# Optimization experiments

Hardware: AMD Instinct MI355X
Metric: run time of the kernel (lower is better)

Reference implementation:

```python
import jax, jax.numpy as jnp
import numpy as np
import math

B, C, H, W = 8, 512, 32, 32
NUM_GROUPS = 32
NUM_HEADS = C // 64  # num_head_channels=64 -> 8 heads
EPS = 1e-5


def setup_inputs() -> dict:
    key = jax.random.key(0)
    ks = jax.random.split(key, 7)
    x = jax.random.normal(ks[0], (B, C, H, W), dtype=jnp.float32)
    gn_w = jax.random.uniform(ks[1], (C,), dtype=jnp.float32, minval=0.5, maxval=1.5)
    gn_b = jax.random.normal(ks[2], (C,), dtype=jnp.float32) * 0.1
    qkv_w = jax.random.normal(ks[3], (3 * C, C), dtype=jnp.float32) * 0.02
    qkv_b = jax.random.normal(ks[4], (3 * C,), dtype=jnp.float32) * 0.02
    proj_w = jax.random.normal(ks[5], (C, C), dtype=jnp.float32) * 0.02
    proj_b = jax.random.normal(ks[6], (C,), dtype=jnp.float32) * 0.02
    return {"x": x, "gn_w": gn_w, "gn_b": gn_b, "qkv_w": qkv_w,
            "qkv_b": qkv_b, "proj_w": proj_w, "proj_b": proj_b}


def _group_norm(x, w, b):
    # x: [B, C, L]
    bb, cc, ll = x.shape
    g = x.reshape(bb, NUM_GROUPS, cc // NUM_GROUPS, ll)
    mean = g.mean(axis=(2, 3), keepdims=True)
    var = g.var(axis=(2, 3), keepdims=True)
    g = (g - mean) * jax.lax.rsqrt(var + EPS)
    return g.reshape(bb, cc, ll) * w[None, :, None] + b[None, :, None]


def reference(x, gn_w, gn_b, qkv_w, qkv_b, proj_w, proj_b):
    b, c, h, w = x.shape
    L = h * w
    xf = x.reshape(b, c, L)
    # 1x1 conv1d QKV on normalized input: weight [3C, C]
    qkv = jnp.einsum('oc,bcl->bol', qkv_w, _group_norm(xf, gn_w, gn_b)) + qkv_b[None, :, None]
    ch = c // NUM_HEADS  # per-head channels
    qkv = qkv.reshape(b * NUM_HEADS, 3 * ch, L)
    q, k, v = qkv[:, :ch], qkv[:, ch:2 * ch], qkv[:, 2 * ch:]
    scale = 1.0 / math.sqrt(math.sqrt(ch))
    # [b*H, T, S] scores, softmax over source dim (computed in fp32 per source)
    weight = jnp.einsum('bct,bcs->bts', q * scale, k * scale)
    weight = jax.nn.softmax(weight.astype(jnp.float32), axis=-1).astype(weight.dtype)
    a = jnp.einsum('bts,bcs->bct', weight, v).reshape(b, c, L)
    hproj = jnp.einsum('oc,bcl->bol', proj_w, a) + proj_b[None, :, None]
    return (xf + hproj).reshape(b, c, h, w)
```

## Files before the change

kernel.cpp:

```cpp
#include <hip/hip_runtime.h>
#include <math.h>

#define BB 8
#define CC 512
#define LL 1024
#define GG 32
#define CPG 16
#define NH 8
#define CH 64

typedef unsigned short ushort_t;
typedef __attribute__((ext_vector_type(8))) short short8;
typedef __attribute__((ext_vector_type(4))) float f32x4;
typedef __attribute__((ext_vector_type(16))) float f32x16;

#define SCALE_Q 0.18033688f

__device__ inline ushort_t f2bf(float f) {
  union { float f; unsigned u; } v;
  v.f = f;
  unsigned r = v.u + 0x7FFFu + ((v.u >> 16) & 1u);
  return (ushort_t)(r >> 16);
}

__device__ inline unsigned pack_bf2(float lo, float hi) {
  return __builtin_amdgcn_perm(__float_as_uint(hi), __float_as_uint(lo),
                               0x07060302u);
}

__device__ inline int swz(int r, int k) {
  return r * 64 + ((((k >> 3) ^ (r & 7)) << 3) | (k & 7));
}

__device__ __forceinline__ void g2l16(const void* g, void* l) {
  __builtin_amdgcn_global_load_lds((const unsigned int*)g, (unsigned int*)l,
                                   16, 0, 0);
}

__global__ __launch_bounds__(256) void pre_kernel(
    const float* __restrict__ x, const float* __restrict__ gn_w,
    const float* __restrict__ gn_b, const float* __restrict__ qkv_w,
    const float* __restrict__ proj_w, float* __restrict__ s_bc,
    float* __restrict__ t_bc, ushort_t* __restrict__ wq,
    ushort_t* __restrict__ wp) {
  if (blockIdx.x < BB * GG) {
    int b = blockIdx.x / GG;
    int g = blockIdx.x % GG;
    const float4* xg4 =
        (const float4*)(x + ((size_t)b * CC + (size_t)g * CPG) * LL);
    float sum = 0.f, sq = 0.f;
#pragma unroll
    for (int i = 0; i < 16; ++i) {
      float4 v = xg4[threadIdx.x + i * 256];
      sum += (v.x + v.y) + (v.z + v.w);
      sq += (v.x * v.x + v.y * v.y) + (v.z * v.z + v.w * v.w);
    }
#pragma unroll
    for (int off = 32; off > 0; off >>= 1) {
      sum += __shfl_down(sum, off);
      sq += __shfl_down(sq, off);
    }
    __shared__ float red[8];
    __shared__ float st[2];
    int wave = threadIdx.x >> 6;
    if ((threadIdx.x & 63) == 0) {
      red[wave] = sum;
      red[4 + wave] = sq;
    }
    __syncthreads();
    if (threadIdx.x == 0) {
      float s = red[0] + red[1] + red[2] + red[3];
      float q = red[4] + red[5] + red[6] + red[7];
      float mean = s * (1.f / (CPG * LL));
      float var = q * (1.f / (CPG * LL)) - mean * mean;
      st[0] = mean;
      st[1] = rsqrtf(var + 1e-5f);
    }
    __syncthreads();
    if (threadIdx.x < CPG) {
      int c = g * CPG + threadIdx.x;
      float w = gn_w[c];
      float sc = st[1] * w;
      s_bc[b * CC + c] = sc;
      t_bc[b * CC + c] = gn_b[c] - st[0] * sc;
    }
  } else {
    int cb = blockIdx.x - BB * GG;
    int idx = (cb * 256 + threadIdx.x) * 4;
    const int N1 = 3 * CC * CC;
    float4 v;
    ushort_t* mat;
    int row, k;
    if (idx < N1) {
      v = *(const float4*)(qkv_w + idx);
      row = idx >> 9;
      k = idx & 511;
      mat = wq + (size_t)row * CC;
    } else {
      int j = idx - N1;
      v = *(const float4*)(proj_w + j);
      row = j >> 9;
      k = j & 511;
      mat = wp + (size_t)row * CC;
    }
    int dcol = (k & ~63) | ((((k >> 3) & 7) ^ (row & 7)) << 3) | (k & 7);
    unsigned lo = f2bf(v.x) | ((unsigned)f2bf(v.y) << 16);
    unsigned hi = f2bf(v.z) | ((unsigned)f2bf(v.w) << 16);
    *(uint2*)(mat + dcol) = make_uint2(lo, hi);
  }
}

__global__ __launch_bounds__(256) void xnt_kernel(
    const float* __restrict__ x, const float* __restrict__ s_bc,
    const float* __restrict__ t_bc, ushort_t* __restrict__ xnT) {
  const int b = blockIdx.z;
  const int c0 = blockIdx.y * 64;
  const int l0 = blockIdx.x * 64;
  const int tid = threadIdx.x;
  __shared__ ushort_t Ts[64 * 72];
#pragma unroll
  for (int r4 = 0; r4 < 4; ++r4) {
    int c_local = (tid >> 4) + r4 * 16;
    int l_local = (tid & 15) * 4;
    int c = c0 + c_local;
    float sc = s_bc[b * CC + c], sh = t_bc[b * CC + c];
    float4 v = *(const float4*)(x + ((size_t)b * CC + c) * LL + l0 + l_local);
    float vv[4] = {v.x, v.y, v.z, v.w};
#pragma unroll
    for (int dl = 0; dl < 4; ++dl) {
      int l = l_local + dl;
      int cs = c_local ^ (((l >> 2) & 7) << 3);
      Ts[l * 72 + cs] = f2bf(vv[dl] * sc + sh);
    }
  }
  __syncthreads();
#pragma unroll
  for (int rep = 0; rep < 2; ++rep) {
    int gid = tid + rep * 256;
    int l = gid >> 3, seg = gid & 7;
    uint4 v = *(const uint4*)&Ts[l * 72 + ((seg * 8) ^ (((l >> 2) & 7) << 3))];
    *(uint4*)(xnT + ((size_t)b * LL + l0 + l) * CC + c0 +
              ((seg ^ (l & 7)) << 3)) = v;
  }
}

__global__ __launch_bounds__(384, 3) void qkv_mfma_kernel(
    const ushort_t* __restrict__ wq, const ushort_t* __restrict__ xnT,
    const float* __restrict__ qkv_b, ushort_t* __restrict__ qT,
    ushort_t* __restrict__ kT, ushort_t* __restrict__ vbuf) {
  const int b = blockIdx.z;
  const int m0 = blockIdx.y * 192;
  const int n0 = blockIdx.x * 128;
  const int tid = threadIdx.x;
  const int w = tid >> 6, lane = tid & 63;
  const int col = lane & 15, quad = lane >> 4;
  const int wm = (w >> 1) * 64, wn = (w & 1) * 64;
  __shared__ ushort_t Smem[2 * 20480];
  f32x4 acc[4][4];
  f32x4 z = {0.f, 0.f, 0.f, 0.f};
#pragma unroll
  for (int i = 0; i < 4; ++i)
#pragma unroll
    for (int j = 0; j < 4; ++j) acc[i][j] = z;

  const ushort_t* arow = wq + (size_t)m0 * CC;
  const ushort_t* brow = xnT + ((size_t)b * LL + n0) * CC;

  auto stage = [&](int bb, int k0) {
    ushort_t* As = Smem + bb * 20480;
    ushort_t* Bs = As + 12288;
#pragma unroll
    for (int j = 0; j < 4; ++j) {
      int e = (j * 6 + w) * 512 + lane * 8;
      g2l16(arow + (size_t)(e >> 6) * CC + k0 + (e & 63),
            As + (j * 6 + w) * 512);
    }
    if (w < 4) {
#pragma unroll
      for (int j = 0; j < 4; ++j) {
        int e = (j * 4 + w) * 512 + lane * 8;
        g2l16(brow + (size_t)(e >> 6) * CC + k0 + (e & 63),
              Bs + (j * 4 + w) * 512);
      }
    }
  };

  stage(0, 0);
  __syncthreads();
  int cur = 0;
  for (int step = 0; step < 8; ++step) {
    if (step < 7) stage(cur ^ 1, (step + 1) * 64);
    const ushort_t* As = Smem + cur * 20480;
    const ushort_t* Bs = As + 12288;
#pragma unroll
    for (int kk = 0; kk < 2; ++kk) {
      short8 af[4], bf[4];
#pragma unroll
      for (int mi = 0; mi < 4; ++mi)
        af[mi] = *(const short8*)&As[swz(wm + mi * 16 + col, kk * 32 + quad * 8)];
#pragma unroll
      for (int ni = 0; ni < 4; ++ni)
        bf[ni] = *(const short8*)&Bs[swz(wn + ni * 16 + col, kk * 32 + quad * 8)];
#pragma unroll
      for (int mi = 0; mi < 4; ++mi)
#pragma unroll
        for (int ni = 0; ni < 4; ++ni)
          acc[mi][ni] = __builtin_amdgcn_mfma_f32_16x16x32_bf16(
              af[mi], bf[ni], acc[mi][ni], 0, 0, 0);
    }
    __syncthreads();
    cur ^= 1;
  }
  const int ci_w = w >> 1;
  ushort_t* Tile = Smem + ci_w * 8192;
  if (ci_w < 2) {
    const float sc = (ci_w == 0) ? SCALE_Q : 1.f;
#pragma unroll
    for (int mi = 0; mi < 4; ++mi) {
      int mg = m0 + wm + mi * 16 + quad * 4;
      float b0 = qkv_b[mg + 0], b1 = qkv_b[mg + 1];
      float b2 = qkv_b[mg + 2], b3 = qkv_b[mg + 3];
      int ch = mi * 16 + quad * 4;
#pragma unroll
      for (int ni = 0; ni < 4; ++ni) {
        int lloc = wn + ni * 16 + col;
        float v0 = (acc[mi][ni][0] + b0) * sc;
        float v1 = (acc[mi][ni][1] + b1) * sc;
        float v2 = (acc[mi][ni][2] + b2) * sc;
        float v3 = (acc[mi][ni][3] + b3) * sc;
        int chs = ch ^ ((lloc & 7) << 3);
        *(uint2*)&Tile[lloc * 64 + chs] =
            make_uint2(pack_bf2(v0, v1), pack_bf2(v2, v3));
      }
    }
  } else {
#pragma unroll
    for (int mi = 0; mi < 4; ++mi)
#pragma unroll
      for (int r = 0; r < 4; ++r) {
        int ch = mi * 16 + quad * 4 + r;
        float bias = qkv_b[m0 + wm + ch];
#pragma unroll
        for (int ni = 0; ni < 4; ++ni) {
          int lloc = wn + ni * 16 + col;
          Tile[ch * 128 + lloc] =
              (ushort_t)(__float_as_uint(acc[mi][ni][r] + bias) >> 16);
        }
      }
  }
  __syncthreads();
  const int head = blockIdx.y;
  const int bh = b * NH + head;
#pragma unroll
  for (int ci = 0; ci < 3; ++ci) {
    ushort_t* T2 = Smem + ci * 8192;
    if (ci < 2) {
      ushort_t* dst = (ci == 0) ? qT : kT;
#pragma unroll
      for (int it = 0; it < 3; ++it) {
        int idx = tid + it * 384;
        if (idx < 1024) {
          int l = idx >> 3, seg = idx & 7;
          uint4 v = *(const uint4*)&T2[l * 64 + seg * 8];
          *(uint4*)(dst + ((size_t)bh * LL + n0 + l) * CH + seg * 8) = v;
        }
      }
    } else {
#pragma unroll
      for (int it = 0; it < 3; ++it) {
        int idx = tid + it * 384;
        if (idx < 1024) {
          int ch = idx >> 4, lseg = idx & 15;
          uint4 v = *(const uint4*)&T2[ch * 128 + lseg * 8];
          int g = lseg & 7, blk = lseg >> 3;
          *(uint4*)(vbuf + ((size_t)bh * CH + ch) * LL + n0 + blk * 64 +
                    ((g ^ (ch & 7)) << 3)) = v;
        }
      }
    }
  }
}

__global__ __launch_bounds__(256) void attn_mfma_kernel(
    const ushort_t* __restrict__ qT, const ushort_t* __restrict__ kT,
    const ushort_t* __restrict__ vbuf, ushort_t* __restrict__ abuf) {
  const int Bx = blockIdx.x;
  const int bh = (Bx & 7) * 8 + ((Bx >> 3) >> 3);
  const int t0g = ((Bx >> 3) & 7) * 128;
  const int b = bh >> 3, h = bh & 7;
  const int tid = threadIdx.x;
  const int w = tid >> 6, lane = tid & 63;
  const int ln31 = lane & 31, hi = lane >> 5;
  __shared__ ushort_t Ksm[2][64 * 64];
  __shared__ ushort_t Vsm[2][64 * 64];

  const ushort_t* kbase = kT + (size_t)bh * LL * CH;
  const ushort_t* vbase = vbuf + (size_t)bh * CH * LL;
  const int eb = w * 1024 + lane * 8;

#pragma unroll
  for (int i = 0; i < 2; ++i) {
    int ee = eb + i * 512;
    g2l16(kbase + ee, &Ksm[0][w * 1024 + i * 512]);
    g2l16(vbase + (size_t)(ee >> 6) * LL + (ee & 63),
          &Vsm[0][w * 1024 + i * 512]);
  }
  const ushort_t* qtile = qT + ((size_t)bh * LL + t0g) * CH;
  short8 bq[4];
#pragma unroll
  for (int j = 0; j < 4; ++j)
    bq[j] = *(const short8*)&qtile[swz(w * 32 + ln31, j * 16 + hi * 8)];

  float m_s = 0.f, lsum = 0.f;
  f32x16 oacc[2];
  f32x16 zz = {0.f, 0.f, 0.f, 0.f, 0.f, 0.f, 0.f, 0.f,
               0.f, 0.f, 0.f, 0.f, 0.f, 0.f, 0.f, 0.f};
  oacc[0] = zz;
  oacc[1] = zz;
  __syncthreads();

  int cur = 0;
  for (int it = 0; it < 16; ++it) {
    if (it < 15) {
      const ushort_t* kn = kbase + (size_t)(it + 1) * 64 * CH;
      const ushort_t* vn = vbase + (it + 1) * 64;
#pragma unroll
      for (int i = 0; i < 2; ++i) {
        int ee = eb + i * 512;
        g2l16(kn + ee, &Ksm[cur ^ 1][w * 1024 + i * 512]);
        g2l16(vn + (size_t)(ee >> 6) * LL + (ee & 63),
              &Vsm[cur ^ 1][w * 1024 + i * 512]);
      }
    }
    const ushort_t* Kc = Ksm[cur];
    const ushort_t* Vc = Vsm[cur];
    f32x16 sacc[2];
    sacc[0] = zz;
    sacc[1] = zz;
    __builtin_amdgcn_s_setprio(1);
#pragma unroll
    for (int sq = 0; sq < 2; ++sq)
#pragma unroll
      for (int j = 0; j < 4; ++j) {
        short8 ak = *(const short8*)&Kc[swz(sq * 32 + ln31, j * 16 + hi * 8)];
        sacc[sq] = __builtin_amdgcn_mfma_f32_32x32x16_bf16(ak, bq[j],
                                                           sacc[sq], 0, 0, 0);
      }
    __builtin_amdgcn_s_setprio(0);
    if (it == 0) {
      float mx = sacc[0][0];
#pragma unroll
      for (int sq = 0; sq < 2; ++sq)
#pragma unroll
        for (int r = 0; r < 16; ++r) mx = fmaxf(mx, sacc[sq][r]);
#pragma unroll
      for (int off = 32; off > 0; off >>= 1) mx = fmaxf(mx, __shfl_xor(mx, off));
      m_s = mx;
    }
    short8 pf[4];
#pragma unroll
    for (int sq = 0; sq < 2; ++sq) {
      float p[16];
#pragma unroll
      for (int r = 0; r < 16; ++r) {
        p[r] = __builtin_amdgcn_exp2f(sacc[sq][r] - m_s);
        lsum += p[r];
      }
      unsigned d0[4], d1[4];
#pragma unroll
      for (int q = 0; q < 4; ++q) {
        d0[q] = pack_bf2(p[q * 4 + 0], p[q * 4 + 1]);
        d1[q] = pack_bf2(p[q * 4 + 2], p[q * 4 + 3]);
      }
#pragma unroll
      for (int m = 0; m < 2; ++m) {
        unsigned x0 = d0[m * 2], y0 = d0[m * 2 + 1];
        unsigned x1 = d1[m * 2], y1 = d1[m * 2 + 1];
        asm volatile("v_permlane32_swap_b32 %0, %1" : "+v"(x0), "+v"(y0));
        asm volatile("v_permlane32_swap_b32 %0, %1" : "+v"(x1), "+v"(y1));
        union { uint4 u; short8 s; } fu;
        fu.u = make_uint4(x0, x1, y0, y1);
        pf[sq * 2 + m] = fu.s;
      }
    }
    __builtin_amdgcn_s_setprio(1);
#pragma unroll
    for (int cq = 0; cq < 2; ++cq)
#pragma unroll
      for (int ks = 0; ks < 4; ++ks) {
        short8 bv = *(const short8*)&Vc[swz(cq * 32 + ln31, ks * 16 + hi * 8)];
        oacc[cq] = __builtin_amdgcn_mfma_f32_32x32x16_bf16(pf[ks], bv,
                                                           oacc[cq], 0, 0, 0);
      }
    __builtin_amdgcn_s_setprio(0);
    __syncthreads();
    cur ^= 1;
  }
  lsum += __shfl_xor(lsum, 32);
#pragma unroll
  for (int r = 0; r < 16; ++r) {
    int tl = (r & 3) + 8 * (r >> 2) + 4 * hi;
    float li = 1.f / __shfl(lsum, tl, 64);
    int lg = t0g + w * 32 + tl;
#pragma unroll
    for (int cq = 0; cq < 2; ++cq) {
      int cl = cq * 32 + ln31;
      int dcol = ((((cl >> 3) ^ (lg & 7)) << 3) | (cl & 7));
      abuf[((size_t)b * LL + lg) * CC + h * CH + dcol] =
          f2bf(oacc[cq][r] * li);
    }
  }
}

__global__ __launch_bounds__(256) void proj_mfma_kernel(
    const ushort_t* __restrict__ wp, const ushort_t* __restrict__ abuf,
    const float* __restrict__ proj_b, const float* __restrict__ x,
    float* __restrict__ out) {
  const int b = blockIdx.z;
  const int m0 = blockIdx.y * 64;
  const int n0 = blockIdx.x * 128;
  const int tid = threadIdx.x;
  const int w = tid >> 6, lane = tid & 63;
  const int col = lane & 15, quad = lane >> 4;
  const int wm = (w >> 1) * 32, wn = (w & 1) * 64;
  __shared__ ushort_t Smem[2 * 12288];
  f32x4 acc[2][4];
  f32x4 z = {0.f, 0.f, 0.f, 0.f};
#pragma unroll
  for (int i = 0; i < 2; ++i)
#pragma unroll
    for (int j = 0; j < 4; ++j) acc[i][j] = z;

  const ushort_t* arow = wp + (size_t)m0 * CC;
  const ushort_t* brow = abuf + ((size_t)b * LL + n0) * CC;

  auto stage = [&](int bb, int k0) {
    ushort_t* As = Smem + bb * 12288;
    ushort_t* Bs = As + 4096;
#pragma unroll
    for (int j = 0; j < 2; ++j) {
      int e = (j * 4 + w) * 512 + lane * 8;
      g2l16(arow + (size_t)(e >> 6) * CC + k0 + (e & 63),
            As + (j * 4 + w) * 512);
    }
#pragma unroll
    for (int j = 0; j < 4; ++j) {
      int e = (j * 4 + w) * 512 + lane * 8;
      g2l16(brow + (size_t)(e >> 6) * CC + k0 + (e & 63),
            Bs + (j * 4 + w) * 512);
    }
  };

  stage(0, 0);
  __syncthreads();
  int cur = 0;
  for (int step = 0; step < 8; ++step) {
    if (step < 7) stage(cur ^ 1, (step + 1) * 64);
    const ushort_t* As = Smem + cur * 12288;
    const ushort_t* Bs = As + 4096;
#pragma unroll
    for (int kk = 0; kk < 2; ++kk) {
      short8 af[2], bf[4];
#pragma unroll
      for (int mi = 0; mi < 2; ++mi)
        af[mi] = *(const short8*)&As[swz(wm + mi * 16 + col, kk * 32 + quad * 8)];
#pragma unroll
      for (int ni = 0; ni < 4; ++ni)
        bf[ni] = *(const short8*)&Bs[swz(wn + ni * 16 + col, kk * 32 + quad * 8)];
#pragma unroll
      for (int mi = 0; mi < 2; ++mi)
#pragma unroll
        for (int ni = 0; ni < 4; ++ni)
          acc[mi][ni] = __builtin_amdgcn_mfma_f32_16x16x32_bf16(
              af[mi], bf[ni], acc[mi][ni], 0, 0, 0);
    }
    __syncthreads();
    cur ^= 1;
  }
#pragma unroll
  for (int mi = 0; mi < 2; ++mi)
#pragma unroll
    for (int r = 0; r < 4; ++r) {
      int o = m0 + wm + mi * 16 + quad * 4 + r;
      float bias = proj_b[o];
#pragma unroll
      for (int ni = 0; ni < 4; ++ni) {
        int l = n0 + wn + ni * 16 + col;
        size_t off = ((size_t)b * CC + o) * LL + l;
        out[off] = x[off] + bias + acc[mi][ni][r];
      }
    }
}

extern "C" void kernel_launch(void* const* d_in, const int* in_sizes, int n_in,
                              void* d_out, int out_size, void* d_ws,
                              size_t ws_size, hipStream_t stream) {
  const float* x = (const float*)d_in[0];
  const float* gn_w = (const float*)d_in[1];
  const float* gn_b = (const float*)d_in[2];
  const float* qkv_w = (const float*)d_in[3];
  const float* qkv_b = (const float*)d_in[4];
  const float* proj_w = (const float*)d_in[5];
  const float* proj_b = (const float*)d_in[6];
  float* out = (float*)d_out;

  char* ws = (char*)d_ws;
  float* s_bc = (float*)ws;
  float* t_bc = s_bc + BB * CC;
  ushort_t* wq = (ushort_t*)(t_bc + BB * CC);
  ushort_t* wp = wq + (size_t)3 * CC * CC;
  ushort_t* xnT = wp + (size_t)CC * CC;
  ushort_t* qT = xnT + (size_t)BB * LL * CC;
  ushort_t* kT = qT + (size_t)BB * NH * LL * CH;
  ushort_t* vb = kT + (size_t)BB * NH * LL * CH;
  ushort_t* abuf = vb + (size_t)BB * NH * LL * CH;

  pre_kernel<<<BB * GG + 1024, 256, 0, stream>>>(x, gn_w, gn_b, qkv_w, proj_w,
                                                 s_bc, t_bc, wq, wp);
  xnt_kernel<<<dim3(LL / 64, CC / 64, BB), 256, 0, stream>>>(x, s_bc, t_bc,
                                                             xnT);
  qkv_mfma_kernel<<<dim3(LL / 128, 1536 / 192, BB), 384, 0, stream>>>(
      wq, xnT, qkv_b, qT, kT, vb);
  attn_mfma_kernel<<<dim3(512), 256, 0, stream>>>(qT, kT, vb, abuf);
  proj_mfma_kernel<<<dim3(LL / 128, CC / 64, BB), 256, 0, stream>>>(
      wp, abuf, proj_b, x, out);
}
```

Before: 139.5 us.

## Fuse group-norm stats with normalize-transpose and double attention query tile per block

```diff
diff --git a/kernel.cpp b/kernel.cpp
--- a/kernel.cpp
+++ b/kernel.cpp
@@ -37,56 +37,85 @@
                                    16, 0, 0);
 }
 
-__global__ __launch_bounds__(256) void pre_kernel(
+__global__ __launch_bounds__(512) void gnx_kernel(
     const float* __restrict__ x, const float* __restrict__ gn_w,
     const float* __restrict__ gn_b, const float* __restrict__ qkv_w,
-    const float* __restrict__ proj_w, float* __restrict__ s_bc,
-    float* __restrict__ t_bc, ushort_t* __restrict__ wq,
-    ushort_t* __restrict__ wp) {
+    const float* __restrict__ proj_w, ushort_t* __restrict__ xnT,
+    ushort_t* __restrict__ wq, ushort_t* __restrict__ wp) {
   if (blockIdx.x < BB * GG) {
-    int b = blockIdx.x / GG;
-    int g = blockIdx.x % GG;
-    const float4* xg4 =
-        (const float4*)(x + ((size_t)b * CC + (size_t)g * CPG) * LL);
+    const int b = blockIdx.x / GG;
+    const int g = blockIdx.x % GG;
+    const int tid = threadIdx.x;
+    const int ch = tid >> 5;
+    const int lseg = tid & 31;
+    __shared__ ushort_t Ts[1024 * 32];
+    __shared__ float red[16];
+    __shared__ float st[2];
+    const float* xc = x + ((size_t)b * CC + (size_t)g * CPG + ch) * LL;
+    float4 v[8];
     float sum = 0.f, sq = 0.f;
 #pragma unroll
-    for (int i = 0; i < 16; ++i) {
-      float4 v = xg4[threadIdx.x + i * 256];
-      sum += (v.x + v.y) + (v.z + v.w);
-      sq += (v.x * v.x + v.y * v.y) + (v.z * v.z + v.w * v.w);
+    for (int i = 0; i < 8; ++i) {
+      v[i] = *(const float4*)(xc + lseg * 32 + i * 4);
+      sum += (v[i].x + v[i].y) + (v[i].z + v[i].w);
+      sq += (v[i].x * v[i].x + v[i].y * v[i].y) +
+            (v[i].z * v[i].z + v[i].w * v[i].w);
     }
 #pragma unroll
     for (int off = 32; off > 0; off >>= 1) {
       sum += __shfl_down(sum, off);
       sq += __shfl_down(sq, off);
     }
-    __shared__ float red[8];
-    __shared__ float st[2];
-    int wave = threadIdx.x >> 6;
-    if ((threadIdx.x & 63) == 0) {
+    const int wave = tid >> 6;
+    if ((tid & 63) == 0) {
       red[wave] = sum;
-      red[4 + wave] = sq;
+      red[8 + wave] = sq;
     }
     __syncthreads();
-    if (threadIdx.x == 0) {
-      float s = red[0] + red[1] + red[2] + red[3];
-      float q = red[4] + red[5] + red[6] + red[7];
+    if (tid == 0) {
+      float s = 0.f, q = 0.f;
+#pragma unroll
+      for (int i = 0; i < 8; ++i) {
+        s += red[i];
+        q += red[8 + i];
+      }
       float mean = s * (1.f / (CPG * LL));
       float var = q * (1.f / (CPG * LL)) - mean * mean;
       st[0] = mean;
       st[1] = rsqrtf(var + 1e-5f);
     }
     __syncthreads();
-    if (threadIdx.x < CPG) {
-      int c = g * CPG + threadIdx.x;
-      float w = gn_w[c];
-      float sc = st[1] * w;
-      s_bc[b * CC + c] = sc;
-      t_bc[b * CC + c] = gn_b[c] - st[0] * sc;
+    const int c = g * CPG + ch;
+    const float sc = st[1] * gn_w[c];
+    const float sh = gn_b[c] - st[0] * sc;
+    const int chG = ch >> 3, ch7 = ch & 7;
+#pragma unroll
+    for (int i = 0; i < 8; ++i) {
+      float vv[4] = {v[i].x, v[i].y, v[i].z, v[i].w};
+#pragma unroll
+      for (int j = 0; j < 4; ++j) {
+        int l = lseg * 32 + i * 4 + j;
+        int key = ((l >> 5) + (l >> 2)) & 3;
+        int slot = (chG + key) & 3;
+        Ts[l * 32 + slot * 8 + ch7] = f2bf(vv[j] * sc + sh);
+      }
+    }
+    __syncthreads();
+    const int cb64 = (g >> 2) * 64;
+    const int grpb = (g & 3) * 2;
+#pragma unroll
+    for (int it = 0; it < 4; ++it) {
+      int idx = tid + it * 512;
+      int l = idx >> 1, gsel = idx & 1;
+      int key = ((l >> 5) + (l >> 2)) & 3;
+      int slot = (gsel + key) & 3;
+      uint4 val = *(const uint4*)&Ts[l * 32 + slot * 8];
+      int grp = (grpb + gsel) ^ (l & 7);
+      *(uint4*)(xnT + ((size_t)b * LL + l) * CC + cb64 + grp * 8) = val;
     }
   } else {
     int cb = blockIdx.x - BB * GG;
-    int idx = (cb * 256 + threadIdx.x) * 4;
+    int idx = (cb * 512 + threadIdx.x) * 4;
     const int N1 = 3 * CC * CC;
     float4 v;
     ushort_t* mat;
@@ -110,40 +139,6 @@
   }
 }
 
-__global__ __launch_bounds__(256) void xnt_kernel(
-    const float* __restrict__ x, const float* __restrict__ s_bc,
-    const float* __restrict__ t_bc, ushort_t* __restrict__ xnT) {
-  const int b = blockIdx.z;
-  const int c0 = blockIdx.y * 64;
-  const int l0 = blockIdx.x * 64;
-  const int tid = threadIdx.x;
-  __shared__ ushort_t Ts[64 * 72];
-#pragma unroll
-  for (int r4 = 0; r4 < 4; ++r4) {
-    int c_local = (tid >> 4) + r4 * 16;
-    int l_local = (tid & 15) * 4;
-    int c = c0 + c_local;
-    float sc = s_bc[b * CC + c], sh = t_bc[b * CC + c];
-    float4 v = *(const float4*)(x + ((size_t)b * CC + c) * LL + l0 + l_local);
-    float vv[4] = {v.x, v.y, v.z, v.w};
-#pragma unroll
-    for (int dl = 0; dl < 4; ++dl) {
-      int l = l_local + dl;
-      int cs = c_local ^ (((l >> 2) & 7) << 3);
-      Ts[l * 72 + cs] = f2bf(vv[dl] * sc + sh);
-    }
-  }
-  __syncthreads();
-#pragma unroll
-  for (int rep = 0; rep < 2; ++rep) {
-    int gid = tid + rep * 256;
-    int l = gid >> 3, seg = gid & 7;
-    uint4 v = *(const uint4*)&Ts[l * 72 + ((seg * 8) ^ (((l >> 2) & 7) << 3))];
-    *(uint4*)(xnT + ((size_t)b * LL + l0 + l) * CC + c0 +
-              ((seg ^ (l & 7)) << 3)) = v;
-  }
-}
-
 __global__ __launch_bounds__(384, 3) void qkv_mfma_kernel(
     const ushort_t* __restrict__ wq, const ushort_t* __restrict__ xnT,
     const float* __restrict__ qkv_b, ushort_t* __restrict__ qT,
@@ -281,12 +276,12 @@
   }
 }
 
-__global__ __launch_bounds__(256) void attn_mfma_kernel(
+__global__ __launch_bounds__(512) void attn_mfma_kernel(
     const ushort_t* __restrict__ qT, const ushort_t* __restrict__ kT,
     const ushort_t* __restrict__ vbuf, ushort_t* __restrict__ abuf) {
   const int Bx = blockIdx.x;
-  const int bh = (Bx & 7) * 8 + ((Bx >> 3) >> 3);
-  const int t0g = ((Bx >> 3) & 7) * 128;
+  const int bh = (Bx & 7) * 8 + ((Bx >> 3) >> 2);
+  const int t0g = ((Bx >> 3) & 3) * 256;
   const int b = bh >> 3, h = bh & 7;
   const int tid = threadIdx.x;
   const int w = tid >> 6, lane = tid & 63;
@@ -296,15 +291,10 @@
 
   const ushort_t* kbase = kT + (size_t)bh * LL * CH;
   const ushort_t* vbase = vbuf + (size_t)bh * CH * LL;
-  const int eb = w * 1024 + lane * 8;
-
-#pragma unroll
-  for (int i = 0; i < 2; ++i) {
-    int ee = eb + i * 512;
-    g2l16(kbase + ee, &Ksm[0][w * 1024 + i * 512]);
-    g2l16(vbase + (size_t)(ee >> 6) * LL + (ee & 63),
-          &Vsm[0][w * 1024 + i * 512]);
-  }
+  const int eb = w * 512 + lane * 8;
+
+  g2l16(kbase + eb, &Ksm[0][w * 512]);
+  g2l16(vbase + (size_t)(eb >> 6) * LL + (eb & 63), &Vsm[0][w * 512]);
   const ushort_t* qtile = qT + ((size_t)bh * LL + t0g) * CH;
   short8 bq[4];
 #pragma unroll
@@ -322,15 +312,9 @@
   int cur = 0;
   for (int it = 0; it < 16; ++it) {
     if (it < 15) {
-      const ushort_t* kn = kbase + (size_t)(it + 1) * 64 * CH;
-      const ushort_t* vn = vbase + (it + 1) * 64;
-#pragma unroll
-      for (int i = 0; i < 2; ++i) {
-        int ee = eb + i * 512;
-        g2l16(kn + ee, &Ksm[cur ^ 1][w * 1024 + i * 512]);
-        g2l16(vn + (size_t)(ee >> 6) * LL + (ee & 63),
-              &Vsm[cur ^ 1][w * 1024 + i * 512]);
-      }
+      g2l16(kbase + (size_t)(it + 1) * 64 * CH + eb, &Ksm[cur ^ 1][w * 512]);
+      g2l16(vbase + (size_t)(eb >> 6) * LL + (it + 1) * 64 + (eb & 63),
+            &Vsm[cur ^ 1][w * 512]);
     }
     const ushort_t* Kc = Ksm[cur];
     const ushort_t* Vc = Vsm[cur];
@@ -505,9 +489,7 @@
   float* out = (float*)d_out;
 
   char* ws = (char*)d_ws;
-  float* s_bc = (float*)ws;
-  float* t_bc = s_bc + BB * CC;
-  ushort_t* wq = (ushort_t*)(t_bc + BB * CC);
+  ushort_t* wq = (ushort_t*)ws;
   ushort_t* wp = wq + (size_t)3 * CC * CC;
   ushort_t* xnT = wp + (size_t)CC * CC;
   ushort_t* qT = xnT + (size_t)BB * LL * CC;
@@ -515,13 +497,11 @@
   ushort_t* vb = kT + (size_t)BB * NH * LL * CH;
   ushort_t* abuf = vb + (size_t)BB * NH * LL * CH;
 
-  pre_kernel<<<BB * GG + 1024, 256, 0, stream>>>(x, gn_w, gn_b, qkv_w, proj_w,
-                                                 s_bc, t_bc, wq, wp);
-  xnt_kernel<<<dim3(LL / 64, CC / 64, BB), 256, 0, stream>>>(x, s_bc, t_bc,
-                                                             xnT);
+  gnx_kernel<<<BB * GG + 512, 512, 0, stream>>>(x, gn_w, gn_b, qkv_w, proj_w,
+                                                xnT, wq, wp);
   qkv_mfma_kernel<<<dim3(LL / 128, 1536 / 192, BB), 384, 0, stream>>>(
       wq, xnT, qkv_b, qT, kT, vb);
-  attn_mfma_kernel<<<dim3(512), 256, 0, stream>>>(qT, kT, vb, abuf);
+  attn_mfma_kernel<<<dim3(256), 512, 0, stream>>>(qT, kT, vb, abuf);
   proj_mfma_kernel<<<dim3(LL / 128, CC / 64, BB), 256, 0, stream>>>(
       wp, abuf, proj_b, x, out);
 }
```

After: 140.1 us. Within noise of the previous version (+0.4%).
